# Performance work log

Measured on AMD Instinct MI355X. Metric: run time of the kernel, lower is better.

The kernel has to match this reference:

```python
import jax, jax.numpy as jnp
import numpy as np

L = 8          # num_layers
H = 1024       # hidden_size
F = 4096       # features_per_layer
B, S = 2, 1024 # batch, seq_len
P = L * (L + 1) // 2  # number of (layer -> target_layer) decoders


def setup_inputs() -> dict:
    key = jax.random.key(0)
    k0, k1, k2, k3 = jax.random.split(key, 4)
    res = jax.random.normal(k0, (L, B, S, H), jnp.float32)          # residual stream per layer
    We = jax.random.normal(k1, (L, F, H), jnp.float32) / np.sqrt(H)  # stacked encoder weights
    be = jnp.zeros((L, F), jnp.float32)
    Wd = jax.random.normal(k2, (P, H, F), jnp.float32) / np.sqrt(F)  # flattened decoder weights, pair (l,t>=l)
    bd = jnp.zeros((P, H), jnp.float32)
    thresh = jnp.full((L,), 0.03, jnp.float32)                       # JumpReLU thresholds
    return {"res": res, "We": We, "be": be, "Wd": Wd, "bd": bd, "thresh": thresh}


def reference(res, We, be, Wd, bd, thresh):
    # Encoders + JumpReLU (eval-mode: x * (x > threshold)) for all layers at once
    preact = jnp.einsum('lbsh,lfh->lbsf', res, We) + be[:, None, None, :]
    feats = jnp.where(preact > thresh[:, None, None, None], preact, jnp.zeros((), preact.dtype))

    # Cross-layer decoders: layer l writes to all targets t >= l (grouped GEMM per source layer)
    recon = jnp.zeros_like(res)
    for l in range(L):
        start = l * L - l * (l - 1) // 2
        k = L - l
        Wl = Wd[start:start + k]           # [k, H, F]
        bl = bd[start:start + k]           # [k, H]
        out = jnp.einsum('bsf,khf->kbsh', feats[l], Wl) + bl[:, None, None, :]
        recon = recon.at[l:].add(out)
    return recon, feats
```

## Files before the change

kernel.cpp:

```cpp
#include <hip/hip_runtime.h>


#define MT 2048
#define HD 1024
#define FD 4096
#define LL 8

typedef __attribute__((ext_vector_type(8))) short short8;
typedef __attribute__((ext_vector_type(4))) float f32x4;
typedef __attribute__((ext_vector_type(4))) unsigned short ushort4v;

typedef const __attribute__((address_space(1))) void GV;
typedef __attribute__((address_space(3))) void LV;

__device__ __forceinline__ void gload16(const void* g, void* l) {
  __builtin_amdgcn_global_load_lds((GV*)g, (LV*)l, 16, 0, 0);
}

#define BAR()                                  \
  do {                                         \
    __builtin_amdgcn_sched_barrier(0);         \
    __builtin_amdgcn_s_barrier();              \
    __builtin_amdgcn_sched_barrier(0);         \
  } while (0)

__device__ __forceinline__ unsigned int f2bf1(float x) {
  unsigned u = __float_as_uint(x);
  return (u + 0x7FFFu + ((u >> 16) & 1u)) >> 16;
}

__device__ __forceinline__ void load_tile(const float* __restrict__ base, int ld,
                                          float4* r) {
  const int t = threadIdx.x;
#pragma unroll
  for (int i = 0; i < 8; ++i) {
    int idx = t + 256 * i;
    int row = idx >> 4;
    int c4  = idx & 15;
    r[i] = *(const float4*)(base + (size_t)row * ld + c4 * 4);
  }
}

__device__ __forceinline__ void write_tile(char* lds, const float4* r) {
  const int t = threadIdx.x;
#pragma unroll
  for (int i = 0; i < 8; ++i) {
    int idx = t + 256 * i;
    int row = idx >> 4;
    int c4  = idx & 15;
    int off = (row * 128 + c4 * 8) ^ ((row & 7) << 4);
    unsigned lo = f2bf1(r[i].x) | (f2bf1(r[i].y) << 16);
    unsigned hi = f2bf1(r[i].z) | (f2bf1(r[i].w) << 16);
    *(uint2*)(lds + off) = make_uint2(lo, hi);
  }
}

__device__ __forceinline__ void load_tile_bf(const unsigned short* __restrict__ base,
                                             int ld, short8* r) {
  const int t = threadIdx.x;
#pragma unroll
  for (int i = 0; i < 4; ++i) {
    int idx = t + 256 * i;
    int row = idx >> 3;
    int c8  = idx & 7;
    r[i] = *(const short8*)(base + (size_t)row * ld + c8 * 8);
  }
}

__device__ __forceinline__ void write_tile_bf(char* lds, const short8* r) {
  const int t = threadIdx.x;
#pragma unroll
  for (int i = 0; i < 4; ++i) {
    int idx = t + 256 * i;
    int row = idx >> 3;
    int c8  = idx & 7;
    int off = (row * 128 + c8 * 16) ^ ((row & 7) << 4);
    *(short8*)(lds + off) = r[i];
  }
}

__device__ __forceinline__ void compute_tile(const char* sA, const char* sB,
                                             f32x4 acc[4][4], int wr, int wc,
                                             int l16, int h16) {
#pragma unroll
  for (int ks = 0; ks < 2; ++ks) {
    short8 a[4], b[4];
#pragma unroll
    for (int i = 0; i < 4; ++i) {
      int row = wr * 64 + i * 16 + l16;
      a[i] = *(const short8*)(sA + ((row * 128 + ks * 64 + h16 * 16) ^ ((row & 7) << 4)));
    }
#pragma unroll
    for (int j = 0; j < 4; ++j) {
      int col = wc * 64 + j * 16 + l16;
      b[j] = *(const short8*)(sB + ((col * 128 + ks * 64 + h16 * 16) ^ ((col & 7) << 4)));
    }
#pragma unroll
    for (int i = 0; i < 4; ++i)
#pragma unroll
      for (int j = 0; j < 4; ++j)
        acc[i][j] = __builtin_amdgcn_mfma_f32_16x16x32_bf16(a[i], b[j], acc[i][j], 0, 0, 0);
  }
}

__global__ __launch_bounds__(256) void conv_kernel(
    const float* __restrict__ res, const float* __restrict__ We,
    const float* __restrict__ Wd, unsigned short* __restrict__ res_bf,
    unsigned short* __restrict__ we_bf, unsigned short* __restrict__ wd_bf) {
  const size_t stride = (size_t)gridDim.x * 256;
  const size_t i0 = (size_t)blockIdx.x * 256 + threadIdx.x;
  auto cv = [&](const float* __restrict__ s, unsigned short* __restrict__ d,
                size_t n4) {
    const float4* s4 = (const float4*)s;
    for (size_t k = i0; k < n4; k += stride) {
      float4 v = s4[k];
      ushort4v o;
      o.x = (unsigned short)f2bf1(v.x);
      o.y = (unsigned short)f2bf1(v.y);
      o.z = (unsigned short)f2bf1(v.z);
      o.w = (unsigned short)f2bf1(v.w);
      *(ushort4v*)(d + k * 4) = o;
    }
  };
  cv(res, res_bf, (size_t)LL * MT * HD / 4);
  cv(We,  we_bf,  (size_t)LL * FD * HD / 4);
  cv(Wd,  wd_bf,  (size_t)36 * HD * FD / 4);
}

__global__ __launch_bounds__(256, 2) void enc_kernel(
    const float* __restrict__ res, const float* __restrict__ We,
    const float* __restrict__ be, const float* __restrict__ thresh,
    float* __restrict__ feats, unsigned short* __restrict__ feats_bf,
    const float* __restrict__ wd_src, unsigned short* __restrict__ wd_dst,
    int conv_z) {
  __shared__ char sA[128 * 64 * 2];
  __shared__ char sB[128 * 64 * 2];

  if ((int)blockIdx.z < conv_z) {
    size_t chunk = ((size_t)blockIdx.z * 16 + blockIdx.y) * 32 + blockIdx.x;
    size_t base = chunk * 36864 + threadIdx.x;
    const float4* src = (const float4*)wd_src;
#pragma unroll 4
    for (int i = 0; i < 144; ++i) {
      size_t k = base + (size_t)i * 256;
      float4 v = src[k];
      ushort4v o;
      o.x = (unsigned short)f2bf1(v.x);
      o.y = (unsigned short)f2bf1(v.y);
      o.z = (unsigned short)f2bf1(v.z);
      o.w = (unsigned short)f2bf1(v.w);
      *(ushort4v*)(wd_dst + k * 4) = o;
    }
    return;
  }

  const int l  = blockIdx.z - conv_z;
  const int m0 = blockIdx.y * 128;
  const int f0 = blockIdx.x * 128;

  const float* Abase = res + (size_t)l * MT * HD + (size_t)m0 * HD;
  const float* Bbase = We  + (size_t)l * FD * HD + (size_t)f0 * HD;

  const int t = threadIdx.x;
  const int lane = t & 63, wave = t >> 6;
  const int wr = wave >> 1, wc = wave & 1;
  const int l16 = lane & 15, h16 = lane >> 4;

  f32x4 acc[4][4];
#pragma unroll
  for (int i = 0; i < 4; ++i)
#pragma unroll
    for (int j = 0; j < 4; ++j) acc[i][j] = (f32x4){0.f, 0.f, 0.f, 0.f};

  float4 ra[8], rb[8];
  load_tile(Abase, HD, ra);
  load_tile(Bbase, HD, rb);

  const int NK = HD / 64;
  for (int kt = 0; kt < NK; ++kt) {
    write_tile(sA, ra);
    write_tile(sB, rb);
    __syncthreads();
    if (kt + 1 < NK) {
      load_tile(Abase + (kt + 1) * 64, HD, ra);
      load_tile(Bbase + (kt + 1) * 64, HD, rb);
    }
    compute_tile(sA, sB, acc, wr, wc, l16, h16);
    __syncthreads();
  }

  const float th = thresh[l];
#pragma unroll
  for (int j = 0; j < 4; ++j) {
    int col = f0 + wc * 64 + j * 16 + l16;
    float bev = be[(size_t)l * FD + col];
#pragma unroll
    for (int i = 0; i < 4; ++i) {
      int rbase = m0 + wr * 64 + i * 16 + h16 * 4;
#pragma unroll
      for (int q = 0; q < 4; ++q) {
        float v = acc[i][j][q] + bev;
        float g = (v > th) ? v : 0.f;
        size_t idx = ((size_t)l * MT + rbase + q) * FD + col;
        feats[idx] = g;
        if (feats_bf) feats_bf[idx] = (unsigned short)f2bf1(g);
      }
    }
  }
}

#define DEC_ABUF 32768
#define DEC_BUFSZ 49152
__global__ __launch_bounds__(512, 2) void enc8(
    const unsigned short* __restrict__ resbf,
    const unsigned short* __restrict__ webf,
    const float* __restrict__ be, const float* __restrict__ thresh,
    float* __restrict__ feats, unsigned short* __restrict__ feats_bf) {
  __shared__ char lds[3 * DEC_BUFSZ];

  const int flat = (int)(blockIdx.x + 32 * blockIdx.y + 256 * blockIdx.z);
  const int nf = (flat & 7) * 256 + (flat >> 3);
  const int bx = nf & 31;
  const int by = (nf >> 5) & 7;
  const int l  = nf >> 8;

  const int m0 = by * 256;
  const int f0 = bx * 128;

  const int t = threadIdx.x;
  const int L = t & 63;
  const int w = t >> 6;
  const int wm = w >> 1, wn = w & 1;
  const int l16 = L & 15, h16 = L >> 4;

  const int rl   = (t >> 3) & 7;
  const int scol = (t & 7) ^ rl;
  const int rowl = t >> 3;
  const unsigned short* Abase = resbf + (size_t)l * MT * HD;
  const unsigned short* Bbase = webf + (size_t)l * FD * HD;
  const size_t laneA = (size_t)(m0 + rowl) * HD + scol * 8;
  const size_t laneB = (size_t)(f0 + rowl) * HD + scol * 8;

  const int s0 = h16 ^ (l16 & 7);
  const int NT = HD / 64;

  f32x4 acc[4][4];
#pragma unroll
  for (int i = 0; i < 4; ++i)
#pragma unroll
    for (int j = 0; j < 4; ++j) acc[i][j] = (f32x4){0.f, 0.f, 0.f, 0.f};

  auto stage = [&](int bi, int tt) {
    const unsigned short* Ab = Abase + (size_t)tt * 64 + laneA;
    const unsigned short* Bb = Bbase + (size_t)tt * 64 + laneB;
    char* dA = lds + bi * DEC_BUFSZ + t * 16;
    char* dB = dA + DEC_ABUF;
#pragma unroll
    for (int i = 0; i < 4; ++i)
      gload16(Ab + (size_t)i * 64 * HD, dA + i * 8192);
#pragma unroll
    for (int i = 0; i < 2; ++i)
      gload16(Bb + (size_t)i * 64 * HD, dB + i * 8192);
  };

  auto rfrag = [&](int bi, int ks, short8* a, short8* b) {
    const char* cA = lds + bi * DEC_BUFSZ;
    const char* cB = cA + DEC_ABUF;
    const int sl = (s0 ^ (ks << 2)) << 4;
#pragma unroll
    for (int i = 0; i < 4; ++i) {
      int row = wm * 64 + i * 16 + l16;
      a[i] = *(const short8*)(cA + row * 128 + sl);
    }
#pragma unroll
    for (int j = 0; j < 4; ++j) {
      int col = wn * 64 + j * 16 + l16;
      b[j] = *(const short8*)(cB + col * 128 + sl);
    }
  };

  auto cluster = [&](const short8* a, const short8* b) {
    __builtin_amdgcn_s_setprio(1);
#pragma unroll
    for (int i = 0; i < 4; ++i)
#pragma unroll
      for (int j = 0; j < 4; ++j)
        acc[i][j] = __builtin_amdgcn_mfma_f32_16x16x32_bf16(a[i], b[j], acc[i][j], 0, 0, 0);
    __builtin_amdgcn_s_setprio(0);
  };

  stage(0, 0);
  stage(1, 1);
  asm volatile("s_waitcnt vmcnt(6)" ::: "memory");
  BAR();

  short8 aC[4], bC[4], aN[4], bN[4];
  rfrag(0, 0, aC, bC);

  int rd = 0;
  for (int tt = 0; tt < NT; ++tt) {
    int st = rd + 2;
    if (st >= 3) st -= 3;
    if (tt + 2 < NT) stage(st, tt + 2);
    rfrag(rd, 1, aN, bN);
    cluster(aC, bC);
    if (tt + 2 < NT) {
      asm volatile("s_waitcnt vmcnt(6)" ::: "memory");
    } else if (tt + 1 < NT) {
      asm volatile("s_waitcnt vmcnt(0)" ::: "memory");
    }
    BAR();
    int nrd = (rd + 1 == 3) ? 0 : rd + 1;
    if (tt + 1 < NT) rfrag(nrd, 0, aC, bC);
    cluster(aN, bN);
    rd = nrd;
  }

  const float th = thresh[l];
#pragma unroll
  for (int j = 0; j < 4; ++j) {
    int col = f0 + wn * 64 + j * 16 + l16;
    float bev = be[(size_t)l * FD + col];
#pragma unroll
    for (int i = 0; i < 4; ++i) {
      int rbase = m0 + wm * 64 + i * 16 + h16 * 4;
#pragma unroll
      for (int q = 0; q < 4; ++q) {
        float v = acc[i][j][q] + bev;
        float g = (v > th) ? v : 0.f;
        size_t idx = ((size_t)l * MT + rbase + q) * FD + col;
        feats[idx] = g;
        feats_bf[idx] = (unsigned short)f2bf1(g);
      }
    }
  }
}

__global__ __launch_bounds__(512, 2) void dec8(
    const unsigned short* __restrict__ featsbf,
    const unsigned short* __restrict__ wdbf,
    const float* __restrict__ bd, float* __restrict__ recon) {
  __shared__ char lds[3 * DEC_BUFSZ];

  const int flat = (int)(blockIdx.x + 8 * blockIdx.y + 64 * blockIdx.z);
  const int nf = (flat & 7) * 32 + (flat >> 3);
  const int bx = nf & 7;
  const int by = (nf >> 3) & 7;
  const int z  = nf >> 6;

  const int m0 = by * 256;
  const int h0 = bx * 128;

  const int t = threadIdx.x;
  const int L = t & 63;
  const int w = t >> 6;
  const int wm = w >> 1, wn = w & 1;
  const int l16 = L & 15, h16 = L >> 4;

  const int rl   = (t >> 3) & 7;
  const int scol = (t & 7) ^ rl;
  const int rowl = t >> 3;
  const size_t laneA = (size_t)(m0 + rowl) * FD + scol * 8;
  const size_t laneB = (size_t)(h0 + rowl) * FD + scol * 8;

  const int s0 = h16 ^ (l16 & 7);

  for (int sub = 0; sub < 2; ++sub) {
    const int lp = sub ? z : 7 - z;
    const int NT = (lp + 1) * 64;

    f32x4 acc[4][4];
#pragma unroll
    for (int i = 0; i < 4; ++i)
#pragma unroll
      for (int j = 0; j < 4; ++j) acc[i][j] = (f32x4){0.f, 0.f, 0.f, 0.f};

    auto stage = [&](int bi, int tt) {
      int l = tt >> 6, kt = tt & 63;
      int p = l * LL - ((l * (l - 1)) >> 1) + (lp - l);
      const unsigned short* Ab = featsbf + (size_t)l * MT * FD + kt * 64 + laneA;
      const unsigned short* Bb = wdbf + (size_t)p * HD * FD + kt * 64 + laneB;
      char* dA = lds + bi * DEC_BUFSZ + t * 16;
      char* dB = dA + DEC_ABUF;
#pragma unroll
      for (int i = 0; i < 4; ++i)
        gload16(Ab + (size_t)i * 64 * FD, dA + i * 8192);
#pragma unroll
      for (int i = 0; i < 2; ++i)
        gload16(Bb + (size_t)i * 64 * FD, dB + i * 8192);
    };

    auto rfrag = [&](int bi, int ks, short8* a, short8* b) {
      const char* cA = lds + bi * DEC_BUFSZ;
      const char* cB = cA + DEC_ABUF;
      const int sl = (s0 ^ (ks << 2)) << 4;
#pragma unroll
      for (int i = 0; i < 4; ++i) {
        int row = wm * 64 + i * 16 + l16;
        a[i] = *(const short8*)(cA + row * 128 + sl);
      }
#pragma unroll
      for (int j = 0; j < 4; ++j) {
        int col = wn * 64 + j * 16 + l16;
        b[j] = *(const short8*)(cB + col * 128 + sl);
      }
    };

    auto cluster = [&](const short8* a, const short8* b) {
      __builtin_amdgcn_s_setprio(1);
#pragma unroll
      for (int i = 0; i < 4; ++i)
#pragma unroll
        for (int j = 0; j < 4; ++j)
          acc[i][j] = __builtin_amdgcn_mfma_f32_16x16x32_bf16(a[i], b[j], acc[i][j], 0, 0, 0);
      __builtin_amdgcn_s_setprio(0);
    };

    stage(0, 0);
    stage(1, 1);
    asm volatile("s_waitcnt vmcnt(6)" ::: "memory");
    BAR();

    short8 aC[4], bC[4], aN[4], bN[4];
    rfrag(0, 0, aC, bC);

    int rd = 0;
    for (int tt = 0; tt < NT; ++tt) {
      int st = rd + 2;
      if (st >= 3) st -= 3;
      if (tt + 2 < NT) stage(st, tt + 2);
      rfrag(rd, 1, aN, bN);
      cluster(aC, bC);
      if (tt + 2 < NT) {
        asm volatile("s_waitcnt vmcnt(6)" ::: "memory");
      } else if (tt + 1 < NT) {
        asm volatile("s_waitcnt vmcnt(0)" ::: "memory");
      }
      BAR();
      int nrd = (rd + 1 == 3) ? 0 : rd + 1;
      if (tt + 1 < NT) rfrag(nrd, 0, aC, bC);
      cluster(aN, bN);
      rd = nrd;
    }

#pragma unroll
    for (int j = 0; j < 4; ++j) {
      int col = h0 + wn * 64 + j * 16 + l16;
      float bsum = 0.f;
      for (int l = 0; l <= lp; ++l) {
        int p = l * LL - ((l * (l - 1)) >> 1) + (lp - l);
        bsum += bd[(size_t)p * HD + col];
      }
#pragma unroll
      for (int i = 0; i < 4; ++i) {
        int rbase = m0 + wm * 64 + i * 16 + h16 * 4;
#pragma unroll
        for (int q = 0; q < 4; ++q)
          recon[((size_t)lp * MT + rbase + q) * HD + col] = acc[i][j][q] + bsum;
      }
    }
  }
}

template <bool ABF16>
__global__ __launch_bounds__(256, 2) void dec_kernel(
    const float* __restrict__ feats_f32, const unsigned short* __restrict__ feats_bf,
    const float* __restrict__ Wd, const float* __restrict__ bd,
    float* __restrict__ recon) {
  __shared__ char sA[128 * 64 * 2];
  __shared__ char sB[128 * 64 * 2];

  const int lp = (LL - 1) - (int)blockIdx.z;
  const int m0 = blockIdx.y * 128;
  const int h0 = blockIdx.x * 128;

  const int t = threadIdx.x;
  const int lane = t & 63, wave = t >> 6;
  const int wr = wave >> 1, wc = wave & 1;
  const int l16 = lane & 15, h16 = lane >> 4;

  f32x4 acc[4][4];
#pragma unroll
  for (int i = 0; i < 4; ++i)
#pragma unroll
    for (int j = 0; j < 4; ++j) acc[i][j] = (f32x4){0.f, 0.f, 0.f, 0.f};

  const int nit = (lp + 1) * (FD / 64);

  auto Abf = [&](int it) -> const unsigned short* {
    int l = it >> 6, kt = it & 63;
    return feats_bf + ((size_t)l * MT + m0) * FD + kt * 64;
  };
  auto Af = [&](int it) -> const float* {
    int l = it >> 6, kt = it & 63;
    return feats_f32 + ((size_t)l * MT + m0) * FD + kt * 64;
  };
  auto Bb = [&](int it) -> const float* {
    int l = it >> 6, kt = it & 63;
    int p = l * LL - l * (l - 1) / 2 + (lp - l);
    return Wd + ((size_t)p * HD + h0) * FD + kt * 64;
  };

  short8 rab[4];
  float4 raf[8];
  float4 rb[8];
  if constexpr (ABF16) load_tile_bf(Abf(0), FD, rab); else load_tile(Af(0), FD, raf);
  load_tile(Bb(0), FD, rb);

  for (int it = 0; it < nit; ++it) {
    if constexpr (ABF16) write_tile_bf(sA, rab); else write_tile(sA, raf);
    write_tile(sB, rb);
    __syncthreads();
    if (it + 1 < nit) {
      if constexpr (ABF16) load_tile_bf(Abf(it + 1), FD, rab);
      else                 load_tile(Af(it + 1), FD, raf);
      load_tile(Bb(it + 1), FD, rb);
    }
    compute_tile(sA, sB, acc, wr, wc, l16, h16);
    __syncthreads();
  }

#pragma unroll
  for (int j = 0; j < 4; ++j) {
    int col = h0 + wc * 64 + j * 16 + l16;
    float bsum = 0.f;
    for (int l = 0; l <= lp; ++l) {
      int p = l * LL - l * (l - 1) / 2 + (lp - l);
      bsum += bd[(size_t)p * HD + col];
    }
#pragma unroll
    for (int i = 0; i < 4; ++i) {
      int rbase = m0 + wr * 64 + i * 16 + h16 * 4;
#pragma unroll
      for (int q = 0; q < 4; ++q) {
        recon[((size_t)lp * MT + rbase + q) * HD + col] = acc[i][j][q] + bsum;
      }
    }
  }
}

extern "C" void kernel_launch(void* const* d_in, const int* in_sizes, int n_in,
                              void* d_out, int out_size, void* d_ws, size_t ws_size,
                              hipStream_t stream) {
  const float* res    = (const float*)d_in[0];
  const float* We     = (const float*)d_in[1];
  const float* be     = (const float*)d_in[2];
  const float* Wd     = (const float*)d_in[3];
  const float* bd     = (const float*)d_in[4];
  const float* thresh = (const float*)d_in[5];

  float* recon = (float*)d_out;
  float* feats = recon + (size_t)LL * MT * HD;

  const size_t featsbf_b = (size_t)LL * MT * FD * 2;
  const size_t wdbf_b    = (size_t)36 * HD * FD * 2;
  const size_t resbf_b   = (size_t)LL * MT * HD * 2;
  const size_t webf_b    = (size_t)LL * FD * HD * 2;

  const bool use_bf   = ws_size >= featsbf_b;
  const bool use_full = ws_size >= featsbf_b + wdbf_b;
  const bool use_v3   = ws_size >= featsbf_b + wdbf_b + resbf_b + webf_b;

  unsigned short* feats_bf = (unsigned short*)d_ws;
  unsigned short* wd_bf    = (unsigned short*)((char*)d_ws + featsbf_b);
  unsigned short* res_bf   = (unsigned short*)((char*)d_ws + featsbf_b + wdbf_b);
  unsigned short* we_bf    = (unsigned short*)((char*)d_ws + featsbf_b + wdbf_b + resbf_b);

  if (use_v3) {
    conv_kernel<<<dim3(2048), dim3(256), 0, stream>>>(res, We, Wd, res_bf, we_bf, wd_bf);
    enc8<<<dim3(32, 8, 8), dim3(512), 0, stream>>>(res_bf, we_bf, be, thresh,
                                                   feats, feats_bf);
    dec8<<<dim3(8, 8, 4), dim3(512), 0, stream>>>(feats_bf, wd_bf, bd, recon);
  } else if (use_full) {
    enc_kernel<<<dim3(32, 16, LL + 2), dim3(256), 0, stream>>>(
        res, We, be, thresh, feats, feats_bf, Wd, wd_bf, 2);
    dec8<<<dim3(8, 8, 4), dim3(512), 0, stream>>>(feats_bf, wd_bf, bd, recon);
  } else if (use_bf) {
    enc_kernel<<<dim3(32, 16, LL), dim3(256), 0, stream>>>(
        res, We, be, thresh, feats, feats_bf, nullptr, nullptr, 0);
    dec_kernel<true><<<dim3(8, 16, LL), dim3(256), 0, stream>>>(
        feats, feats_bf, Wd, bd, recon);
  } else {
    enc_kernel<<<dim3(32, 16, LL), dim3(256), 0, stream>>>(
        res, We, be, thresh, feats, nullptr, nullptr, nullptr, 0);
    dec_kernel<false><<<dim3(8, 16, LL), dim3(256), 0, stream>>>(
        feats, nullptr, Wd, bd, recon);
  }
}
```

Measured before the change: 1.003 ms.

## Fold decoder weight bf16 conversion into encoder GEMM grid as interleaved blocks

Moves the fp32-to-bf16 conversion of the decoder weights out of the standalone conversion kernel and into the encoder kernel's grid. Every ninth block converts a slice of Wd instead of computing a GEMM tile. The aim is to overlap this memory-bound conversion with the compute-bound encoder GEMM. The risk is that the conversion blocks compete for bandwidth and occupancy slots with the GEMM tiles, and the new flat-grid remapping changes tile scheduling order.

After: 1.013 ms. About the same (+1.1%).

```diff
diff --git a/kernel.cpp b/kernel.cpp
--- a/kernel.cpp
+++ b/kernel.cpp
@@ -103,10 +103,9 @@
   }
 }
 
-__global__ __launch_bounds__(256) void conv_kernel(
+__global__ __launch_bounds__(256) void conv1(
     const float* __restrict__ res, const float* __restrict__ We,
-    const float* __restrict__ Wd, unsigned short* __restrict__ res_bf,
-    unsigned short* __restrict__ we_bf, unsigned short* __restrict__ wd_bf) {
+    unsigned short* __restrict__ res_bf, unsigned short* __restrict__ we_bf) {
   const size_t stride = (size_t)gridDim.x * 256;
   const size_t i0 = (size_t)blockIdx.x * 256 + threadIdx.x;
   auto cv = [&](const float* __restrict__ s, unsigned short* __restrict__ d,
@@ -124,7 +123,6 @@
   };
   cv(res, res_bf, (size_t)LL * MT * HD / 4);
   cv(We,  we_bf,  (size_t)LL * FD * HD / 4);
-  cv(Wd,  wd_bf,  (size_t)36 * HD * FD / 4);
 }
 
 __global__ __launch_bounds__(256, 2) void enc_kernel(
@@ -215,11 +213,32 @@
     const unsigned short* __restrict__ resbf,
     const unsigned short* __restrict__ webf,
     const float* __restrict__ be, const float* __restrict__ thresh,
-    float* __restrict__ feats, unsigned short* __restrict__ feats_bf) {
+    float* __restrict__ feats, unsigned short* __restrict__ feats_bf,
+    const float* __restrict__ wd_src, unsigned short* __restrict__ wd_dst) {
   __shared__ char lds[3 * DEC_BUFSZ];
 
-  const int flat = (int)(blockIdx.x + 32 * blockIdx.y + 256 * blockIdx.z);
-  const int nf = (flat & 7) * 256 + (flat >> 3);
+  const int flat = (int)blockIdx.x;
+  const int r9 = flat % 9;
+  if (r9 == 8) {
+    const int cid = flat / 9;
+    const float4* src = (const float4*)wd_src;
+    size_t base = (size_t)cid * 147456 + threadIdx.x;
+#pragma unroll 4
+    for (int i = 0; i < 288; ++i) {
+      size_t k = base + (size_t)i * 512;
+      float4 v = src[k];
+      ushort4v o;
+      o.x = (unsigned short)f2bf1(v.x);
+      o.y = (unsigned short)f2bf1(v.y);
+      o.z = (unsigned short)f2bf1(v.z);
+      o.w = (unsigned short)f2bf1(v.w);
+      *(ushort4v*)(wd_dst + k * 4) = o;
+    }
+    return;
+  }
+
+  const int eid = (flat / 9) * 8 + r9;
+  const int nf = (eid & 7) * 256 + (eid >> 3);
   const int bx = nf & 31;
   const int by = (nf >> 5) & 7;
   const int l  = nf >> 8;
@@ -567,9 +586,9 @@
   unsigned short* we_bf    = (unsigned short*)((char*)d_ws + featsbf_b + wdbf_b + resbf_b);
 
   if (use_v3) {
-    conv_kernel<<<dim3(2048), dim3(256), 0, stream>>>(res, We, Wd, res_bf, we_bf, wd_bf);
-    enc8<<<dim3(32, 8, 8), dim3(512), 0, stream>>>(res_bf, we_bf, be, thresh,
-                                                   feats, feats_bf);
+    conv1<<<dim3(1024), dim3(256), 0, stream>>>(res, We, res_bf, we_bf);
+    enc8<<<dim3(2304), dim3(512), 0, stream>>>(res_bf, we_bf, be, thresh,
+                                               feats, feats_bf, Wd, wd_bf);
     dec8<<<dim3(8, 8, 4), dim3(512), 0, stream>>>(feats_bf, wd_bf, bd, recon);
   } else if (use_full) {
     enc_kernel<<<dim3(32, 16, LL + 2), dim3(256), 0, stream>>>(
```

## Fold Wd bf16 conversion into encoder grid and shrink K-tile for higher occupancy

Applied to the files above, without the earlier changes.

The Wd fp32-to-bf16 conversion moves out of the standalone conversion kernel and is interleaved into the encoder launch. Every third block converts a chunk of Wd, so that memory-bound work overlaps with the encoder's MFMA work. Both the encoder and decoder GEMMs switch from a 64-wide to a 32-wide K tile with smaller LDS buffers, allowing four blocks per CU instead of two. The decoder now runs one target layer per block over a flat 512-block grid instead of pairing heavy and light layers, which risks load imbalance and more barriers per FLOP.

New measurement: 1.199 ms. 19.6% more time.

```diff
diff --git a/kernel.cpp b/kernel.cpp
--- a/kernel.cpp
+++ b/kernel.cpp
@@ -103,10 +103,9 @@
   }
 }
 
-__global__ __launch_bounds__(256) void conv_kernel(
+__global__ __launch_bounds__(256) void conv1(
     const float* __restrict__ res, const float* __restrict__ We,
-    const float* __restrict__ Wd, unsigned short* __restrict__ res_bf,
-    unsigned short* __restrict__ we_bf, unsigned short* __restrict__ wd_bf) {
+    unsigned short* __restrict__ res_bf, unsigned short* __restrict__ we_bf) {
   const size_t stride = (size_t)gridDim.x * 256;
   const size_t i0 = (size_t)blockIdx.x * 256 + threadIdx.x;
   auto cv = [&](const float* __restrict__ s, unsigned short* __restrict__ d,
@@ -124,25 +123,141 @@
   };
   cv(res, res_bf, (size_t)LL * MT * HD / 4);
   cv(We,  we_bf,  (size_t)LL * FD * HD / 4);
-  cv(Wd,  wd_bf,  (size_t)36 * HD * FD / 4);
-}
-
-__global__ __launch_bounds__(256, 2) void enc_kernel(
-    const float* __restrict__ res, const float* __restrict__ We,
+}
+
+#define DBUF 24576
+
+__global__ __launch_bounds__(512, 4) void dec8(
+    const unsigned short* __restrict__ featsbf,
+    const unsigned short* __restrict__ wdbf,
+    const float* __restrict__ bd, float* __restrict__ recon) {
+  __shared__ char lds[3 * DBUF];
+
+  const int f = (int)blockIdx.x;
+  const int lp = 7 - (f >> 6);
+  const int g = f & 63;
+  const int m0 = (g >> 3) * 256;
+  const int h0 = (g & 7) * 128;
+
+  const int t = threadIdx.x;
+  const int L = t & 63, w = t >> 6;
+  const int wm = w >> 1, wn = w & 1;
+  const int l16 = L & 15, h16 = L >> 4;
+
+  const int sl   = (t & 7) ^ ((t >> 3) & 7);
+  const int mloc = 2 * (t >> 3) + (sl >> 2);
+  const int koff = (sl & 3) * 8;
+  const size_t laneA = (size_t)(m0 + mloc) * FD + koff;
+  const size_t laneB = (size_t)(h0 + mloc) * FD + koff;
+
+  const int NT = (lp + 1) * 128;
+
+  f32x4 acc[4][4];
+#pragma unroll
+  for (int i = 0; i < 4; ++i)
+#pragma unroll
+    for (int j = 0; j < 4; ++j) acc[i][j] = (f32x4){0.f, 0.f, 0.f, 0.f};
+
+  auto stage = [&](int bi, int tt) {
+    int l = tt >> 7, kt = tt & 127;
+    int p = l * LL - ((l * (l - 1)) >> 1) + (lp - l);
+    const unsigned short* Ab = featsbf + (size_t)l * MT * FD + kt * 32 + laneA;
+    const unsigned short* Bb = wdbf + (size_t)p * HD * FD + kt * 32 + laneB;
+    char* dA = lds + bi * DBUF + t * 16;
+    gload16(Ab, dA);
+    gload16(Ab + (size_t)128 * FD, dA + 8192);
+    gload16(Bb, dA + 16384);
+  };
+
+  auto rfrag = [&](int bi, short8* a, short8* b) {
+    const char* cA = lds + bi * DBUF;
+    const char* cB = cA + 16384;
+#pragma unroll
+    for (int i = 0; i < 4; ++i) {
+      int m = wm * 64 + i * 16 + l16;
+      int p = m >> 1;
+      int s = (((m & 1) << 2) | h16) ^ (p & 7);
+      a[i] = *(const short8*)(cA + p * 128 + s * 16);
+    }
+#pragma unroll
+    for (int j = 0; j < 4; ++j) {
+      int c = wn * 64 + j * 16 + l16;
+      int p = c >> 1;
+      int s = (((c & 1) << 2) | h16) ^ (p & 7);
+      b[j] = *(const short8*)(cB + p * 128 + s * 16);
+    }
+  };
+
+  auto cluster = [&](const short8* a, const short8* b) {
+    __builtin_amdgcn_s_setprio(1);
+#pragma unroll
+    for (int i = 0; i < 4; ++i)
+#pragma unroll
+      for (int j = 0; j < 4; ++j)
+        acc[i][j] = __builtin_amdgcn_mfma_f32_16x16x32_bf16(a[i], b[j], acc[i][j], 0, 0, 0);
+    __builtin_amdgcn_s_setprio(0);
+  };
+
+  stage(0, 0);
+  stage(1, 1);
+  asm volatile("s_waitcnt vmcnt(3)" ::: "memory");
+  BAR();
+
+  short8 aC[4], bC[4];
+  rfrag(0, aC, bC);
+
+  int rd = 0;
+  for (int tt = 0; tt < NT; ++tt) {
+    int st = rd + 2;
+    if (st >= 3) st -= 3;
+    if (tt + 2 < NT) stage(st, tt + 2);
+    cluster(aC, bC);
+    if (tt + 2 < NT) {
+      asm volatile("s_waitcnt vmcnt(3)" ::: "memory");
+    } else if (tt + 1 < NT) {
+      asm volatile("s_waitcnt vmcnt(0)" ::: "memory");
+    }
+    BAR();
+    int nrd = (rd + 1 == 3) ? 0 : rd + 1;
+    if (tt + 1 < NT) rfrag(nrd, aC, bC);
+    rd = nrd;
+  }
+
+#pragma unroll
+  for (int j = 0; j < 4; ++j) {
+    int col = h0 + wn * 64 + j * 16 + l16;
+    float bsum = 0.f;
+    for (int l = 0; l <= lp; ++l) {
+      int p = l * LL - ((l * (l - 1)) >> 1) + (lp - l);
+      bsum += bd[(size_t)p * HD + col];
+    }
+#pragma unroll
+    for (int i = 0; i < 4; ++i) {
+      int rbase = m0 + wm * 64 + i * 16 + h16 * 4;
+#pragma unroll
+      for (int q = 0; q < 4; ++q)
+        recon[((size_t)lp * MT + rbase + q) * HD + col] = acc[i][j][q] + bsum;
+    }
+  }
+}
+
+__global__ __launch_bounds__(512, 4) void enc8(
+    const unsigned short* __restrict__ resbf,
+    const unsigned short* __restrict__ webf,
     const float* __restrict__ be, const float* __restrict__ thresh,
     float* __restrict__ feats, unsigned short* __restrict__ feats_bf,
-    const float* __restrict__ wd_src, unsigned short* __restrict__ wd_dst,
-    int conv_z) {
-  __shared__ char sA[128 * 64 * 2];
-  __shared__ char sB[128 * 64 * 2];
-
-  if ((int)blockIdx.z < conv_z) {
-    size_t chunk = ((size_t)blockIdx.z * 16 + blockIdx.y) * 32 + blockIdx.x;
-    size_t base = chunk * 36864 + threadIdx.x;
+    const float* __restrict__ wd_src, unsigned short* __restrict__ wd_dst) {
+  __shared__ char lds[3 * DBUF];
+
+  const int flat = (int)blockIdx.x;
+  const int r3 = flat % 3;
+  if (r3 == 2) {
+    const int cid = flat / 3;
     const float4* src = (const float4*)wd_src;
+    size_t base = (size_t)cid * 36864 + threadIdx.x;
 #pragma unroll 4
-    for (int i = 0; i < 144; ++i) {
-      size_t k = base + (size_t)i * 256;
+    for (int i = 0; i < 72; ++i) {
+      size_t k = base + (size_t)i * 512;
       float4 v = src[k];
       ushort4v o;
       o.x = (unsigned short)f2bf1(v.x);
@@ -154,7 +269,127 @@
     return;
   }
 
-  const int l  = blockIdx.z - conv_z;
+  const int eid = (flat / 3) * 2 + r3;
+  const int nf = (eid & 7) * 256 + (eid >> 3);
+  const int bx = nf & 31;
+  const int by = (nf >> 5) & 7;
+  const int l  = nf >> 8;
+
+  const int m0 = by * 256;
+  const int f0 = bx * 128;
+
+  const int t = threadIdx.x;
+  const int L = t & 63, w = t >> 6;
+  const int wm = w >> 1, wn = w & 1;
+  const int l16 = L & 15, h16 = L >> 4;
+
+  const int sl   = (t & 7) ^ ((t >> 3) & 7);
+  const int mloc = 2 * (t >> 3) + (sl >> 2);
+  const int koff = (sl & 3) * 8;
+  const unsigned short* Abase = resbf + (size_t)l * MT * HD;
+  const unsigned short* Bbase = webf + (size_t)l * FD * HD;
+  const size_t laneA = (size_t)(m0 + mloc) * HD + koff;
+  const size_t laneB = (size_t)(f0 + mloc) * HD + koff;
+
+  const int NT = HD / 32;
+
+  f32x4 acc[4][4];
+#pragma unroll
+  for (int i = 0; i < 4; ++i)
+#pragma unroll
+    for (int j = 0; j < 4; ++j) acc[i][j] = (f32x4){0.f, 0.f, 0.f, 0.f};
+
+  auto stage = [&](int bi, int tt) {
+    const unsigned short* Ab = Abase + (size_t)tt * 32 + laneA;
+    const unsigned short* Bb = Bbase + (size_t)tt * 32 + laneB;
+    char* dA = lds + bi * DBUF + t * 16;
+    gload16(Ab, dA);
+    gload16(Ab + (size_t)128 * HD, dA + 8192);
+    gload16(Bb, dA + 16384);
+  };
+
+  auto rfrag = [&](int bi, short8* a, short8* b) {
+    const char* cA = lds + bi * DBUF;
+    const char* cB = cA + 16384;
+#pragma unroll
+    for (int i = 0; i < 4; ++i) {
+      int m = wm * 64 + i * 16 + l16;
+      int p = m >> 1;
+      int s = (((m & 1) << 2) | h16) ^ (p & 7);
+      a[i] = *(const short8*)(cA + p * 128 + s * 16);
+    }
+#pragma unroll
+    for (int j = 0; j < 4; ++j) {
+      int c = wn * 64 + j * 16 + l16;
+      int p = c >> 1;
+      int s = (((c & 1) << 2) | h16) ^ (p & 7);
+      b[j] = *(const short8*)(cB + p * 128 + s * 16);
+    }
+  };
+
+  auto cluster = [&](const short8* a, const short8* b) {
+    __builtin_amdgcn_s_setprio(1);
+#pragma unroll
+    for (int i = 0; i < 4; ++i)
+#pragma unroll
+      for (int j = 0; j < 4; ++j)
+        acc[i][j] = __builtin_amdgcn_mfma_f32_16x16x32_bf16(a[i], b[j], acc[i][j], 0, 0, 0);
+    __builtin_amdgcn_s_setprio(0);
+  };
+
+  stage(0, 0);
+  stage(1, 1);
+  asm volatile("s_waitcnt vmcnt(3)" ::: "memory");
+  BAR();
+
+  short8 aC[4], bC[4];
+  rfrag(0, aC, bC);
+
+  int rd = 0;
+  for (int tt = 0; tt < NT; ++tt) {
+    int st = rd + 2;
+    if (st >= 3) st -= 3;
+    if (tt + 2 < NT) stage(st, tt + 2);
+    cluster(aC, bC);
+    if (tt + 2 < NT) {
+      asm volatile("s_waitcnt vmcnt(3)" ::: "memory");
+    } else if (tt + 1 < NT) {
+      asm volatile("s_waitcnt vmcnt(0)" ::: "memory");
+    }
+    BAR();
+    int nrd = (rd + 1 == 3) ? 0 : rd + 1;
+    if (tt + 1 < NT) rfrag(nrd, aC, bC);
+    rd = nrd;
+  }
+
+  const float th = thresh[l];
+#pragma unroll
+  for (int j = 0; j < 4; ++j) {
+    int col = f0 + wn * 64 + j * 16 + l16;
+    float bev = be[(size_t)l * FD + col];
+#pragma unroll
+    for (int i = 0; i < 4; ++i) {
+      int rbase = m0 + wm * 64 + i * 16 + h16 * 4;
+#pragma unroll
+      for (int q = 0; q < 4; ++q) {
+        float v = acc[i][j][q] + bev;
+        float g = (v > th) ? v : 0.f;
+        size_t idx = ((size_t)l * MT + rbase + q) * FD + col;
+        feats[idx] = g;
+        feats_bf[idx] = (unsigned short)f2bf1(g);
+      }
+    }
+  }
+}
+
+__global__ __launch_bounds__(256, 2) void enc_kernel(
+    const float* __restrict__ res, const float* __restrict__ We,
+    const float* __restrict__ be, const float* __restrict__ thresh,
+    float* __restrict__ feats, unsigned short* __restrict__ feats_bf) {
+  __shared__ char sA[128 * 64 * 2];
+  __shared__ char sB[128 * 64 * 2];
+
+  const int l  = blockIdx.z;
   const int m0 = blockIdx.y * 128;
   const int f0 = blockIdx.x * 128;
 
@@ -204,259 +439,6 @@
         size_t idx = ((size_t)l * MT + rbase + q) * FD + col;
         feats[idx] = g;
         if (feats_bf) feats_bf[idx] = (unsigned short)f2bf1(g);
-      }
-    }
-  }
-}
-
-#define DEC_ABUF 32768
-#define DEC_BUFSZ 49152
-__global__ __launch_bounds__(512, 2) void enc8(
-    const unsigned short* __restrict__ resbf,
-    const unsigned short* __restrict__ webf,
-    const float* __restrict__ be, const float* __restrict__ thresh,
-    float* __restrict__ feats, unsigned short* __restrict__ feats_bf) {
-  __shared__ char lds[3 * DEC_BUFSZ];
-
-  const int flat = (int)(blockIdx.x + 32 * blockIdx.y + 256 * blockIdx.z);
-  const int nf = (flat & 7) * 256 + (flat >> 3);
-  const int bx = nf & 31;
-  const int by = (nf >> 5) & 7;
-  const int l  = nf >> 8;
-
-  const int m0 = by * 256;
-  const int f0 = bx * 128;
-
-  const int t = threadIdx.x;
-  const int L = t & 63;
-  const int w = t >> 6;
-  const int wm = w >> 1, wn = w & 1;
-  const int l16 = L & 15, h16 = L >> 4;
-
-  const int rl   = (t >> 3) & 7;
-  const int scol = (t & 7) ^ rl;
-  const int rowl = t >> 3;
-  const unsigned short* Abase = resbf + (size_t)l * MT * HD;
-  const unsigned short* Bbase = webf + (size_t)l * FD * HD;
-  const size_t laneA = (size_t)(m0 + rowl) * HD + scol * 8;
-  const size_t laneB = (size_t)(f0 + rowl) * HD + scol * 8;
-
-  const int s0 = h16 ^ (l16 & 7);
-  const int NT = HD / 64;
-
-  f32x4 acc[4][4];
-#pragma unroll
-  for (int i = 0; i < 4; ++i)
-#pragma unroll
-    for (int j = 0; j < 4; ++j) acc[i][j] = (f32x4){0.f, 0.f, 0.f, 0.f};
-
-  auto stage = [&](int bi, int tt) {
-    const unsigned short* Ab = Abase + (size_t)tt * 64 + laneA;
-    const unsigned short* Bb = Bbase + (size_t)tt * 64 + laneB;
-    char* dA = lds + bi * DEC_BUFSZ + t * 16;
-    char* dB = dA + DEC_ABUF;
-#pragma unroll
-    for (int i = 0; i < 4; ++i)
-      gload16(Ab + (size_t)i * 64 * HD, dA + i * 8192);
-#pragma unroll
-    for (int i = 0; i < 2; ++i)
-      gload16(Bb + (size_t)i * 64 * HD, dB + i * 8192);
-  };
-
-  auto rfrag = [&](int bi, int ks, short8* a, short8* b) {
-    const char* cA = lds + bi * DEC_BUFSZ;
-    const char* cB = cA + DEC_ABUF;
-    const int sl = (s0 ^ (ks << 2)) << 4;
-#pragma unroll
-    for (int i = 0; i < 4; ++i) {
-      int row = wm * 64 + i * 16 + l16;
-      a[i] = *(const short8*)(cA + row * 128 + sl);
-    }
-#pragma unroll
-    for (int j = 0; j < 4; ++j) {
-      int col = wn * 64 + j * 16 + l16;
-      b[j] = *(const short8*)(cB + col * 128 + sl);
-    }
-  };
-
-  auto cluster = [&](const short8* a, const short8* b) {
-    __builtin_amdgcn_s_setprio(1);
-#pragma unroll
-    for (int i = 0; i < 4; ++i)
-#pragma unroll
-      for (int j = 0; j < 4; ++j)
-        acc[i][j] = __builtin_amdgcn_mfma_f32_16x16x32_bf16(a[i], b[j], acc[i][j], 0, 0, 0);
-    __builtin_amdgcn_s_setprio(0);
-  };
-
-  stage(0, 0);
-  stage(1, 1);
-  asm volatile("s_waitcnt vmcnt(6)" ::: "memory");
-  BAR();
-
-  short8 aC[4], bC[4], aN[4], bN[4];
-  rfrag(0, 0, aC, bC);
-
-  int rd = 0;
-  for (int tt = 0; tt < NT; ++tt) {
-    int st = rd + 2;
-    if (st >= 3) st -= 3;
-    if (tt + 2 < NT) stage(st, tt + 2);
-    rfrag(rd, 1, aN, bN);
-    cluster(aC, bC);
-    if (tt + 2 < NT) {
-      asm volatile("s_waitcnt vmcnt(6)" ::: "memory");
-    } else if (tt + 1 < NT) {
-      asm volatile("s_waitcnt vmcnt(0)" ::: "memory");
-    }
-    BAR();
-    int nrd = (rd + 1 == 3) ? 0 : rd + 1;
-    if (tt + 1 < NT) rfrag(nrd, 0, aC, bC);
-    cluster(aN, bN);
-    rd = nrd;
-  }
-
-  const float th = thresh[l];
-#pragma unroll
-  for (int j = 0; j < 4; ++j) {
-    int col = f0 + wn * 64 + j * 16 + l16;
-    float bev = be[(size_t)l * FD + col];
-#pragma unroll
-    for (int i = 0; i < 4; ++i) {
-      int rbase = m0 + wm * 64 + i * 16 + h16 * 4;
-#pragma unroll
-      for (int q = 0; q < 4; ++q) {
-        float v = acc[i][j][q] + bev;
-        float g = (v > th) ? v : 0.f;
-        size_t idx = ((size_t)l * MT + rbase + q) * FD + col;
-        feats[idx] = g;
-        feats_bf[idx] = (unsigned short)f2bf1(g);
-      }
-    }
-  }
-}
-
-__global__ __launch_bounds__(512, 2) void dec8(
-    const unsigned short* __restrict__ featsbf,
-    const unsigned short* __restrict__ wdbf,
-    const float* __restrict__ bd, float* __restrict__ recon) {
-  __shared__ char lds[3 * DEC_BUFSZ];
-
-  const int flat = (int)(blockIdx.x + 8 * blockIdx.y + 64 * blockIdx.z);
-  const int nf = (flat & 7) * 32 + (flat >> 3);
-  const int bx = nf & 7;
-  const int by = (nf >> 3) & 7;
-  const int z  = nf >> 6;
-
-  const int m0 = by * 256;
-  const int h0 = bx * 128;
-
-  const int t = threadIdx.x;
-  const int L = t & 63;
-  const int w = t >> 6;
-  const int wm = w >> 1, wn = w & 1;
-  const int l16 = L & 15, h16 = L >> 4;
-
-  const int rl   = (t >> 3) & 7;
-  const int scol = (t & 7) ^ rl;
-  const int rowl = t >> 3;
-  const size_t laneA = (size_t)(m0 + rowl) * FD + scol * 8;
-  const size_t laneB = (size_t)(h0 + rowl) * FD + scol * 8;
-
-  const int s0 = h16 ^ (l16 & 7);
-
-  for (int sub = 0; sub < 2; ++sub) {
-    const int lp = sub ? z : 7 - z;
-    const int NT = (lp + 1) * 64;
-
-    f32x4 acc[4][4];
-#pragma unroll
-    for (int i = 0; i < 4; ++i)
-#pragma unroll
-      for (int j = 0; j < 4; ++j) acc[i][j] = (f32x4){0.f, 0.f, 0.f, 0.f};
-
-    auto stage = [&](int bi, int tt) {
-      int l = tt >> 6, kt = tt & 63;
-      int p = l * LL - ((l * (l - 1)) >> 1) + (lp - l);
-      const unsigned short* Ab = featsbf + (size_t)l * MT * FD + kt * 64 + laneA;
-      const unsigned short* Bb = wdbf + (size_t)p * HD * FD + kt * 64 + laneB;
-      char* dA = lds + bi * DEC_BUFSZ + t * 16;
-      char* dB = dA + DEC_ABUF;
-#pragma unroll
-      for (int i = 0; i < 4; ++i)
-        gload16(Ab + (size_t)i * 64 * FD, dA + i * 8192);
-#pragma unroll
-      for (int i = 0; i < 2; ++i)
-        gload16(Bb + (size_t)i * 64 * FD, dB + i * 8192);
-    };
-
-    auto rfrag = [&](int bi, int ks, short8* a, short8* b) {
-      const char* cA = lds + bi * DEC_BUFSZ;
-      const char* cB = cA + DEC_ABUF;
-      const int sl = (s0 ^ (ks << 2)) << 4;
-#pragma unroll
-      for (int i = 0; i < 4; ++i) {
-        int row = wm * 64 + i * 16 + l16;
-        a[i] = *(const short8*)(cA + row * 128 + sl);
-      }
-#pragma unroll
-      for (int j = 0; j < 4; ++j) {
-        int col = wn * 64 + j * 16 + l16;
-        b[j] = *(const short8*)(cB + col * 128 + sl);
-      }
-    };
-
-    auto cluster = [&](const short8* a, const short8* b) {
-      __builtin_amdgcn_s_setprio(1);
-#pragma unroll
-      for (int i = 0; i < 4; ++i)
-#pragma unroll
-        for (int j = 0; j < 4; ++j)
-          acc[i][j] = __builtin_amdgcn_mfma_f32_16x16x32_bf16(a[i], b[j], acc[i][j], 0, 0, 0);
-      __builtin_amdgcn_s_setprio(0);
-    };
-
-    stage(0, 0);
-    stage(1, 1);
-    asm volatile("s_waitcnt vmcnt(6)" ::: "memory");
-    BAR();
-
-    short8 aC[4], bC[4], aN[4], bN[4];
-    rfrag(0, 0, aC, bC);
-
-    int rd = 0;
-    for (int tt = 0; tt < NT; ++tt) {
-      int st = rd + 2;
-      if (st >= 3) st -= 3;
-      if (tt + 2 < NT) stage(st, tt + 2);
-      rfrag(rd, 1, aN, bN);
-      cluster(aC, bC);
-      if (tt + 2 < NT) {
-        asm volatile("s_waitcnt vmcnt(6)" ::: "memory");
-      } else if (tt + 1 < NT) {
-        asm volatile("s_waitcnt vmcnt(0)" ::: "memory");
-      }
-      BAR();
-      int nrd = (rd + 1 == 3) ? 0 : rd + 1;
-      if (tt + 1 < NT) rfrag(nrd, 0, aC, bC);
-      cluster(aN, bN);
-      rd = nrd;
-    }
-
-#pragma unroll
-    for (int j = 0; j < 4; ++j) {
-      int col = h0 + wn * 64 + j * 16 + l16;
-      float bsum = 0.f;
-      for (int l = 0; l <= lp; ++l) {
-        int p = l * LL - ((l * (l - 1)) >> 1) + (lp - l);
-        bsum += bd[(size_t)p * HD + col];
-      }
-#pragma unroll
-      for (int i = 0; i < 4; ++i) {
-        int rbase = m0 + wm * 64 + i * 16 + h16 * 4;
-#pragma unroll
-        for (int q = 0; q < 4; ++q)
-          recon[((size_t)lp * MT + rbase + q) * HD + col] = acc[i][j][q] + bsum;
       }
     }
   }
@@ -557,9 +539,8 @@
   const size_t resbf_b   = (size_t)LL * MT * HD * 2;
   const size_t webf_b    = (size_t)LL * FD * HD * 2;
 
-  const bool use_bf   = ws_size >= featsbf_b;
-  const bool use_full = ws_size >= featsbf_b + wdbf_b;
-  const bool use_v3   = ws_size >= featsbf_b + wdbf_b + resbf_b + webf_b;
+  const bool use_bf = ws_size >= featsbf_b;
+  const bool use_v3 = ws_size >= featsbf_b + wdbf_b + resbf_b + webf_b;
 
   unsigned short* feats_bf = (unsigned short*)d_ws;
   unsigned short* wd_bf    = (unsigned short*)((char*)d_ws + featsbf_b);
@@ -567,22 +548,18 @@
   unsigned short* we_bf    = (unsigned short*)((char*)d_ws + featsbf_b + wdbf_b + resbf_b);
 
   if (use_v3) {
-    conv_kernel<<<dim3(2048), dim3(256), 0, stream>>>(res, We, Wd, res_bf, we_bf, wd_bf);
-    enc8<<<dim3(32, 8, 8), dim3(512), 0, stream>>>(res_bf, we_bf, be, thresh,
-                                                   feats, feats_bf);
-    dec8<<<dim3(8, 8, 4), dim3(512), 0, stream>>>(feats_bf, wd_bf, bd, recon);
-  } else if (use_full) {
-    enc_kernel<<<dim3(32, 16, LL + 2), dim3(256), 0, stream>>>(
-        res, We, be, thresh, feats, feats_bf, Wd, wd_bf, 2);
-    dec8<<<dim3(8, 8, 4), dim3(512), 0, stream>>>(feats_bf, wd_bf, bd, recon);
+    conv1<<<dim3(1024), dim3(256), 0, stream>>>(res, We, res_bf, we_bf);
+    enc8<<<dim3(3072), dim3(512), 0, stream>>>(res_bf, we_bf, be, thresh,
+                                               feats, feats_bf, Wd, wd_bf);
+    dec8<<<dim3(512), dim3(512), 0, stream>>>(feats_bf, wd_bf, bd, recon);
   } else if (use_bf) {
     enc_kernel<<<dim3(32, 16, LL), dim3(256), 0, stream>>>(
-        res, We, be, thresh, feats, feats_bf, nullptr, nullptr, 0);
+        res, We, be, thresh, feats, feats_bf);
     dec_kernel<true><<<dim3(8, 16, LL), dim3(256), 0, stream>>>(
         feats, feats_bf, Wd, bd, recon);
   } else {
     enc_kernel<<<dim3(32, 16, LL), dim3(256), 0, stream>>>(
-        res, We, be, thresh, feats, nullptr, nullptr, nullptr, 0);
+        res, We, be, thresh, feats, nullptr);
     dec_kernel<false><<<dim3(8, 16, LL), dim3(256), 0, stream>>>(
         feats, nullptr, Wd, bd, recon);
   }
```
